# Kernel tuning notes

Measured on AMD Instinct MI355X. Metric: run time of the kernel, lower is better.

The kernel has to match this reference:

```python
import jax, jax.numpy as jnp
import numpy as np

N_NODES = 100000
N_EDGES = 1600000
IN_FEAT = 256
OUT_FEAT = 64


def setup_inputs() -> dict:
    key = jax.random.key(0)
    k1, k2, k3, k4, k5 = jax.random.split(key, 5)
    feat = jax.random.normal(k1, (N_NODES, IN_FEAT), dtype=jnp.float32)
    # Xavier-uniform-like init for the weight
    limit = float(np.sqrt(6.0 / (IN_FEAT + OUT_FEAT)))
    weight = jax.random.uniform(k2, (IN_FEAT, OUT_FEAT), dtype=jnp.float32,
                                minval=-limit, maxval=limit)
    # Sparse adjacency in COO form: rows sorted for segment_sum efficiency
    adj_rows = jnp.sort(jax.random.randint(k3, (N_EDGES,), 0, N_NODES, dtype=jnp.int64))
    adj_cols = jax.random.randint(k4, (N_EDGES,), 0, N_NODES, dtype=jnp.int64)
    adj_vals = jax.random.uniform(k5, (N_EDGES,), dtype=jnp.float32)
    return {"feat": feat, "weight": weight, "adj_rows": adj_rows,
            "adj_cols": adj_cols, "adj_vals": adj_vals}


def reference(feat, weight, adj_rows, adj_cols, adj_vals):
    # out = adj @ (feat @ W), adj sparse COO -> gather + weighted scatter-add
    proj = feat @ weight                       # [N, out_feat] dense mm
    msgs = adj_vals[:, None] * proj[adj_cols]  # [E, out_feat] gather
    out = jax.ops.segment_sum(msgs, adj_rows, num_segments=feat.shape[0],
                              indices_are_sorted=True)
    return out
```

## Files before the change

kernel.cpp:

```cpp
#include <hip/hip_runtime.h>
#include <cstdint>

#define IN_FEAT 256
#define OUT_FEAT 64

constexpr int EPW = 64;

typedef __attribute__((ext_vector_type(4))) float f32x4;
typedef __attribute__((ext_vector_type(8))) _Float16 f16x8;

union HF8 { _Float16 h[8]; f16x8 v; };

__global__ __launch_bounds__(256) void gemm_proj_mfma(
    const float* __restrict__ feat, const float* __restrict__ W,
    _Float16* __restrict__ projh, float* __restrict__ out, int n_rows)
{
    __shared__ _Float16 sWh[8 * 4 * 64 * 8];

    const int lane = threadIdx.x & 63;
    const int wave = threadIdx.x >> 6;
    const int row0 = blockIdx.x * 64 + wave * 16;
    const int kgrp = lane >> 4;
    int ar = row0 + (lane & 15);
    if (ar >= n_rows) ar = n_rows - 1;

    f32x4 fa[16];
    const float* fp = feat + (size_t)ar * IN_FEAT + kgrp * 8;
    #pragma unroll
    for (int ks = 0; ks < 8; ++ks) {
        fa[2 * ks]     = *reinterpret_cast<const f32x4*>(fp + ks * 32);
        fa[2 * ks + 1] = *reinterpret_cast<const f32x4*>(fp + ks * 32 + 4);
    }
    __builtin_amdgcn_sched_barrier(0);

    {
        const int c   = threadIdx.x & 63;
        const int kg0 = threadIdx.x >> 6;
        #pragma unroll
        for (int it = 0; it < 8; ++it) {
            const int kg = it * 4 + kg0;
            HF8 tmp;
            #pragma unroll
            for (int j = 0; j < 8; ++j)
                tmp.h[j] = (_Float16)W[(kg * 8 + j) * OUT_FEAT + c];
            const int ks = kg >> 2;
            const int l  = (kg & 3) * 16 + (c & 15);
            const int ct = c >> 4;
            *reinterpret_cast<f16x8*>(&sWh[((ks * 4 + ct) * 64 + l) * 8]) = tmp.v;
        }
    }
    __syncthreads();
    if (row0 >= n_rows) return;

    f32x4 acc[4];
    #pragma unroll
    for (int ct = 0; ct < 4; ++ct) acc[ct] = f32x4{0.f, 0.f, 0.f, 0.f};

    #pragma unroll
    for (int ks = 0; ks < 8; ++ks) {
        HF8 A;
        #pragma unroll
        for (int h = 0; h < 2; ++h) {
            const f32x4 v = fa[2 * ks + h];
            #pragma unroll
            for (int j = 0; j < 4; ++j)
                A.h[h * 4 + j] = (_Float16)v[j];
        }
        #pragma unroll
        for (int ct = 0; ct < 4; ++ct) {
            HF8 B;
            B.v = *reinterpret_cast<const f16x8*>(
                &sWh[((ks * 4 + ct) * 64 + lane) * 8]);
            acc[ct] = __builtin_amdgcn_mfma_f32_16x16x32_f16(A.v, B.v, acc[ct], 0, 0, 0);
        }
    }

    #pragma unroll
    for (int r = 0; r < 4; ++r) {
        const int row = row0 + kgrp * 4 + r;
        if (row < n_rows) {
            #pragma unroll
            for (int ct = 0; ct < 4; ++ct)
                projh[(size_t)row * OUT_FEAT + ct * 16 + (lane & 15)] =
                    (_Float16)acc[ct][r];
        }
    }

    #pragma unroll
    for (int i = 0; i < 4; ++i) {
        const int row = row0 + i * 4 + (lane >> 4);
        if (row < n_rows)
            *reinterpret_cast<f32x4*>(
                out + (size_t)row * OUT_FEAT + (lane & 15) * 4) =
                f32x4{0.f, 0.f, 0.f, 0.f};
    }
}

__global__ __launch_bounds__(256) void gather_scatter(
    const _Float16* __restrict__ projh, const int* __restrict__ rows,
    const int* __restrict__ cols, const float* __restrict__ vals,
    float* __restrict__ out, int n_edges)
{
    const int lane = threadIdx.x & 63;
    const long wid = (long)((blockIdx.x * 256 + threadIdx.x) >> 6);
    const long e0 = wid * EPW;
    if (e0 >= n_edges) return;

    const long ee = (e0 + lane < n_edges) ? (e0 + lane) : (n_edges - 1);
    const int r_v = rows[ee];
    const int c_v = cols[ee];
    const int v_bits = (e0 + lane < n_edges)
                         ? __builtin_bit_cast(int, vals[ee]) : 0;

    _Float16 p[EPW];
    #pragma unroll
    for (int i = 0; i < EPW; ++i) {
        const int c = __builtin_amdgcn_readlane(c_v, i);
        p[i] = projh[(size_t)c * OUT_FEAT + lane];
    }
    __builtin_amdgcn_sched_barrier(0);

    float acc = 0.f;
    int cur = __builtin_amdgcn_readlane(r_v, 0);
    bool first_seg = true;
    #pragma unroll
    for (int i = 0; i < EPW; ++i) {
        const int   r = __builtin_amdgcn_readlane(r_v, i);
        const float v = __builtin_bit_cast(float, __builtin_amdgcn_readlane(v_bits, i));
        if (r != cur) {
            float* dst = out + (size_t)cur * OUT_FEAT + lane;
            if (first_seg) atomicAdd(dst, acc);
            else           *dst = acc;
            first_seg = false;
            acc = 0.f;
            cur = r;
        }
        acc = fmaf(v, (float)p[i], acc);
    }
    atomicAdd(out + (size_t)cur * OUT_FEAT + lane, acc);
}

extern "C" void kernel_launch(void* const* d_in, const int* in_sizes, int n_in,
                              void* d_out, int out_size, void* d_ws, size_t ws_size,
                              hipStream_t stream)
{
    const float* feat     = (const float*)d_in[0];
    const float* weight   = (const float*)d_in[1];
    const int*   adj_rows = (const int*)d_in[2];
    const int*   adj_cols = (const int*)d_in[3];
    const float* adj_vals = (const float*)d_in[4];
    float*       out      = (float*)d_out;
    _Float16*    projh    = (_Float16*)d_ws;

    const int n_nodes = in_sizes[0] / IN_FEAT;
    const int n_edges = in_sizes[2];

    const int gemm_blocks = (n_nodes + 63) / 64;
    gemm_proj_mfma<<<gemm_blocks, 256, 0, stream>>>(feat, weight, projh, out,
                                                    n_nodes);

    const int waves  = (n_edges + EPW - 1) / EPW;
    const int blocks = (waves + 3) / 4;
    gather_scatter<<<blocks, 256, 0, stream>>>(projh, adj_rows, adj_cols,
                                               adj_vals, out, n_edges);
}
```

Baseline: 61.26 us.

## Switch scatter to row-partitioned CSR traversal with row_ptr built in GEMM kernel

```diff
diff --git a/kernel.cpp b/kernel.cpp
--- a/kernel.cpp
+++ b/kernel.cpp
@@ -4,7 +4,7 @@
 #define IN_FEAT 256
 #define OUT_FEAT 64
 
-constexpr int EPW = 64;
+constexpr int RPW = 16;
 
 typedef __attribute__((ext_vector_type(4))) float f32x4;
 typedef __attribute__((ext_vector_type(8))) _Float16 f16x8;
@@ -13,7 +13,8 @@
 
 __global__ __launch_bounds__(256) void gemm_proj_mfma(
     const float* __restrict__ feat, const float* __restrict__ W,
-    _Float16* __restrict__ projh, float* __restrict__ out, int n_rows)
+    _Float16* __restrict__ projh, const int* __restrict__ rows,
+    int* __restrict__ row_ptr, int n_rows, int n_edges)
 {
     __shared__ _Float16 sWh[8 * 4 * 64 * 8];
 
@@ -32,6 +33,23 @@
         fa[2 * ks + 1] = *reinterpret_cast<const f32x4*>(fp + ks * 32 + 4);
     }
     __builtin_amdgcn_sched_barrier(0);
+
+    {
+        const int tid  = blockIdx.x * 256 + threadIdx.x;
+        const int nthr = gridDim.x * 256;
+        for (int e = tid; e < n_edges; e += nthr) {
+            const int r = rows[e];
+            if (e == 0) {
+                for (int q = 0; q <= r; ++q) row_ptr[q] = 0;
+            } else {
+                const int rp = rows[e - 1];
+                for (int q = rp + 1; q <= r; ++q) row_ptr[q] = e;
+            }
+            if (e == n_edges - 1) {
+                for (int q = r + 1; q <= n_rows; ++q) row_ptr[q] = n_edges;
+            }
+        }
+    }
 
     {
         const int c   = threadIdx.x & 63;
@@ -85,59 +103,66 @@
                     (_Float16)acc[ct][r];
         }
     }
-
-    #pragma unroll
-    for (int i = 0; i < 4; ++i) {
-        const int row = row0 + i * 4 + (lane >> 4);
-        if (row < n_rows)
-            *reinterpret_cast<f32x4*>(
-                out + (size_t)row * OUT_FEAT + (lane & 15) * 4) =
-                f32x4{0.f, 0.f, 0.f, 0.f};
-    }
 }
 
 __global__ __launch_bounds__(256) void gather_scatter(
     const _Float16* __restrict__ projh, const int* __restrict__ rows,
     const int* __restrict__ cols, const float* __restrict__ vals,
-    float* __restrict__ out, int n_edges)
+    const int* __restrict__ row_ptr, float* __restrict__ out, int n_rows)
 {
     const int lane = threadIdx.x & 63;
-    const long wid = (long)((blockIdx.x * 256 + threadIdx.x) >> 6);
-    const long e0 = wid * EPW;
-    if (e0 >= n_edges) return;
+    const int wid  = (blockIdx.x * 256 + threadIdx.x) >> 6;
+    const int r0 = wid * RPW;
+    if (r0 >= n_rows) return;
+    const int r1 = min(r0 + RPW, n_rows);
 
-    const long ee = (e0 + lane < n_edges) ? (e0 + lane) : (n_edges - 1);
-    const int r_v = rows[ee];
-    const int c_v = cols[ee];
-    const int v_bits = (e0 + lane < n_edges)
-                         ? __builtin_bit_cast(int, vals[ee]) : 0;
+    const int e_begin = row_ptr[r0];
+    const int e_end   = row_ptr[r1];
 
-    _Float16 p[EPW];
+    unsigned flushed = 0;
+
+    if (e_begin < e_end) {
+        float acc = 0.f;
+        int cur = rows[e_begin];
+        for (int b = e_begin; b < e_end; b += 64) {
+            const int rem = e_end - b;
+            const int ee = (lane < rem) ? (b + lane) : (e_end - 1);
+            const int r_v = rows[ee];
+            const int c_v = cols[ee];
+            const int v_bits = (lane < rem)
+                                 ? __builtin_bit_cast(int, vals[ee]) : 0;
+
+            _Float16 p[64];
+            #pragma unroll
+            for (int i = 0; i < 64; ++i) {
+                const int c = __builtin_amdgcn_readlane(c_v, i);
+                p[i] = projh[(size_t)c * OUT_FEAT + lane];
+            }
+            __builtin_amdgcn_sched_barrier(0);
+
+            #pragma unroll
+            for (int i = 0; i < 64; ++i) {
+                const int   r = __builtin_amdgcn_readlane(r_v, i);
+                const float v = __builtin_bit_cast(float,
+                                    __builtin_amdgcn_readlane(v_bits, i));
+                if (r != cur) {
+                    out[(size_t)cur * OUT_FEAT + lane] = acc;
+                    flushed |= 1u << (cur - r0);
+                    acc = 0.f;
+                    cur = r;
+                }
+                acc = fmaf(v, (float)p[i], acc);
+            }
+        }
+        out[(size_t)cur * OUT_FEAT + lane] = acc;
+        flushed |= 1u << (cur - r0);
+    }
+
     #pragma unroll
-    for (int i = 0; i < EPW; ++i) {
-        const int c = __builtin_amdgcn_readlane(c_v, i);
-        p[i] = projh[(size_t)c * OUT_FEAT + lane];
+    for (int j = 0; j < RPW; ++j) {
+        if (r0 + j < n_rows && !(flushed & (1u << j)))
+            out[(size_t)(r0 + j) * OUT_FEAT + lane] = 0.f;
     }
-    __builtin_amdgcn_sched_barrier(0);
-
-    float acc = 0.f;
-    int cur = __builtin_amdgcn_readlane(r_v, 0);
-    bool first_seg = true;
-    #pragma unroll
-    for (int i = 0; i < EPW; ++i) {
-        const int   r = __builtin_amdgcn_readlane(r_v, i);
-        const float v = __builtin_bit_cast(float, __builtin_amdgcn_readlane(v_bits, i));
-        if (r != cur) {
-            float* dst = out + (size_t)cur * OUT_FEAT + lane;
-            if (first_seg) atomicAdd(dst, acc);
-            else           *dst = acc;
-            first_seg = false;
-            acc = 0.f;
-            cur = r;
-        }
-        acc = fmaf(v, (float)p[i], acc);
-    }
-    atomicAdd(out + (size_t)cur * OUT_FEAT + lane, acc);
 }
 
 extern "C" void kernel_launch(void* const* d_in, const int* in_sizes, int n_in,
@@ -150,17 +175,22 @@
     const int*   adj_cols = (const int*)d_in[3];
     const float* adj_vals = (const float*)d_in[4];
     float*       out      = (float*)d_out;
-    _Float16*    projh    = (_Float16*)d_ws;
 
     const int n_nodes = in_sizes[0] / IN_FEAT;
     const int n_edges = in_sizes[2];
 
+    _Float16* projh   = (_Float16*)d_ws;
+    int*      row_ptr = (int*)((char*)d_ws +
+                        (size_t)n_nodes * OUT_FEAT * sizeof(_Float16));
+
     const int gemm_blocks = (n_nodes + 63) / 64;
-    gemm_proj_mfma<<<gemm_blocks, 256, 0, stream>>>(feat, weight, projh, out,
-                                                    n_nodes);
+    gemm_proj_mfma<<<gemm_blocks, 256, 0, stream>>>(feat, weight, projh,
+                                                    adj_rows, row_ptr,
+                                                    n_nodes, n_edges);
 
-    const int waves  = (n_edges + EPW - 1) / EPW;
+    const int waves  = (n_nodes + RPW - 1) / RPW;
     const int blocks = (waves + 3) / 4;
     gather_scatter<<<blocks, 256, 0, stream>>>(projh, adj_rows, adj_cols,
-                                               adj_vals, out, n_edges);
+                                               adj_vals, row_ptr, out,
+                                               n_nodes);
 }
```

After: 78.20 us. 1.28x slower.
